# Kernel tuning notes

Hardware: AMD Instinct MI355X
Metric: run time of the kernel (lower is better)

The kernel has to match this reference:

```python
import jax, jax.numpy as jnp
import numpy as np

DIM = 1024
N_HEADS = 16
HEAD_DIM = DIM // N_HEADS


def setup_inputs() -> dict:
    key = jax.random.key(0)
    ks = jax.random.split(key, 5)
    x = jax.random.normal(ks[0], (2, 2048, DIM), dtype=jnp.float32)
    # nn.Linear-style init scale
    s = 1.0 / np.sqrt(DIM)
    W_qkv = jax.random.uniform(ks[1], (DIM, 3 * DIM), jnp.float32, -s, s)
    b_qkv = jax.random.uniform(ks[2], (3 * DIM,), jnp.float32, -s, s)
    W_proj = jax.random.uniform(ks[3], (DIM, DIM), jnp.float32, -s, s)
    b_proj = jax.random.uniform(ks[4], (DIM,), jnp.float32, -s, s)
    return {"x": x, "W_qkv": W_qkv, "b_qkv": b_qkv, "W_proj": W_proj, "b_proj": b_proj}


def reference(x, W_qkv, b_qkv, W_proj, b_proj):
    B, S, D = x.shape
    scale = HEAD_DIM ** -0.5
    qkv = x @ W_qkv + b_qkv                                   # [B,S,3D]
    qkv = qkv.reshape(B, S, 3, N_HEADS, HEAD_DIM)
    q = qkv[:, :, 0].transpose(0, 2, 1, 3)                    # [B,H,S,d]
    k = qkv[:, :, 1].transpose(0, 2, 1, 3)
    v = qkv[:, :, 2].transpose(0, 2, 1, 3)
    attn = jnp.einsum('bhqd,bhkd->bhqk', q, k) * scale        # [B,H,S,S]
    attn = jax.nn.softmax(attn, axis=-1)
    out = jnp.einsum('bhqk,bhkd->bhqd', attn, v)              # [B,H,S,d]
    out = out.transpose(0, 2, 1, 3).reshape(B, S, D)
    return out @ W_proj + b_proj
```

## Files before the change

kernel.cpp:

```cpp
#include <hip/hip_runtime.h>
#include <stdint.h>

typedef unsigned short u16;
typedef __attribute__((ext_vector_type(8))) short bf16x8;
typedef __attribute__((ext_vector_type(4))) float f32x4;
typedef __attribute__((ext_vector_type(16))) float f32x16;
typedef __attribute__((ext_vector_type(4))) u16 us4;
typedef __attribute__((ext_vector_type(8))) u16 us8;

__device__ __forceinline__ u16 f2bf(float f) {
  union { float f; unsigned u; } v; v.f = f;
  unsigned r = v.u + 0x7fffu + ((v.u >> 16) & 1u);
  return (u16)(r >> 16);
}

__device__ __forceinline__ float bf2f(u16 b) {
  union { float f; unsigned u; } v; v.u = ((unsigned)b) << 16;
  return v.f;
}

__device__ __forceinline__ unsigned pkbf(float a, float b) {
  union { float f; unsigned u; } x, y; x.f = a; y.f = b;
  return __builtin_amdgcn_perm(y.u + 0x8000u, x.u + 0x8000u, 0x07060302u);
}

__device__ __forceinline__ float fast_exp2(float x) {
#if __has_builtin(__builtin_amdgcn_exp2f)
  return __builtin_amdgcn_exp2f(x);
#else
  return exp2f(x);
#endif
}

__device__ __forceinline__ void gld16(const void* g, void* l) {
  __builtin_amdgcn_global_load_lds(
      (const __attribute__((address_space(1))) void*)g,
      (__attribute__((address_space(3))) void*)l, 16, 0, 0);
}

__global__ void cvt_kernel(const float* __restrict__ in, u16* __restrict__ out, int n4) {
  int i = blockIdx.x * blockDim.x + threadIdx.x;
  if (i >= n4) return;
  f32x4 v = ((const f32x4*)in)[i];
  us4 r;
#pragma unroll
  for (int j = 0; j < 4; ++j) r[j] = f2bf(v[j]);
  ((us4*)out)[i] = r;
}

__global__ void transw_kernel(const float* __restrict__ in, u16* __restrict__ out, int R, int C) {
  __shared__ u16 tile[32][33];
  const int tx = threadIdx.x & 31, ty = threadIdx.x >> 5;
  const int c0 = blockIdx.x * 32, r0 = blockIdx.y * 32;
#pragma unroll
  for (int j = 0; j < 4; ++j)
    tile[ty + j * 8][tx] = f2bf(in[(size_t)(r0 + ty + j * 8) * C + c0 + tx]);
  __syncthreads();
#pragma unroll
  for (int j = 0; j < 4; ++j)
    out[(size_t)(c0 + ty + j * 8) * R + r0 + tx] = tile[tx][ty + j * 8];
}

__global__ __launch_bounds__(256) void qkv_gemm_kernel(
    const u16* __restrict__ A, const u16* __restrict__ Bt, const float* __restrict__ bias,
    u16* __restrict__ Qb, u16* __restrict__ Kb, u16* __restrict__ Vtb) {
  __shared__ u16 sm[17408];
  u16* As = sm;
  u16* Bs = sm + 4096;
  const int tid = threadIdx.x;
  const int w = tid >> 6, l = tid & 63, quad = l >> 4, lanelo = l & 15;
  const int wr = w >> 1, wc = w & 1;
  const long m0 = (long)blockIdx.x * 128;
  const long n0 = (long)blockIdx.y * 128;

  f32x4 acc[4][4];
#pragma unroll
  for (int i = 0; i < 4; ++i)
#pragma unroll
    for (int j = 0; j < 4; ++j) acc[i][j] = (f32x4){0.f, 0.f, 0.f, 0.f};

  const u16* ag = A + (m0 + w * 32 + (l >> 2)) * 1024 + (l & 3) * 8;
  const u16* bg = Bt + (n0 + w * 32 + (l >> 2)) * 1024 + (l & 3) * 8;
  u16* asl = As + w * 1024;
  u16* bsl = Bs + w * 1024;

  for (int kt = 0; kt < 32; ++kt) {
    const int ko = kt * 32;
    gld16(ag + ko, asl);
    gld16(ag + 16 * 1024 + ko, asl + 512);
    gld16(bg + ko, bsl);
    gld16(bg + 16 * 1024 + ko, bsl + 512);
    __syncthreads();
    bf16x8 af[4], bf[4];
#pragma unroll
    for (int mt = 0; mt < 4; ++mt)
      af[mt] = *(const bf16x8*)(As + (wr * 64 + mt * 16 + lanelo) * 32 + quad * 8);
#pragma unroll
    for (int nt = 0; nt < 4; ++nt)
      bf[nt] = *(const bf16x8*)(Bs + (wc * 64 + nt * 16 + lanelo) * 32 + quad * 8);
#pragma unroll
    for (int mt = 0; mt < 4; ++mt)
#pragma unroll
      for (int nt = 0; nt < 4; ++nt)
        acc[mt][nt] = __builtin_amdgcn_mfma_f32_16x16x32_bf16(af[mt], bf[nt], acc[mt][nt], 0, 0, 0);
    __syncthreads();
  }

  const int t = (int)(n0 >> 10);
  const float scl = (t == 0) ? 0.18033688011112042f : 1.0f;

  float bias_v[4];
#pragma unroll
  for (int nt = 0; nt < 4; ++nt) bias_v[nt] = bias[n0 + wc * 64 + nt * 16 + lanelo];

  u16* Ct = sm;
#pragma unroll
  for (int mt = 0; mt < 4; ++mt)
#pragma unroll
    for (int nt = 0; nt < 4; ++nt)
#pragma unroll
      for (int r = 0; r < 4; ++r)
        Ct[(wr * 64 + mt * 16 + quad * 4 + r) * 136 + wc * 64 + nt * 16 + lanelo] =
            f2bf((acc[mt][nt][r] + bias_v[nt]) * scl);
  __syncthreads();

  const int b = (int)(m0 >> 11);
  const int s0 = (int)(m0 & 2047);
  const int h0 = (int)((n0 & 1023) >> 6);

  if (t < 2) {
    u16* dst = (t == 0) ? Qb : Kb;
#pragma unroll
    for (int p = 0; p < 8; ++p) {
      const int hh = p >> 2;
      const int sl = (p & 3) * 32 + (tid >> 3);
      const int c8 = tid & 7;
      us8 v = *(const us8*)(Ct + sl * 136 + hh * 64 + c8 * 8);
      const int pos = (c8 + sl) & 7;
      const size_t off = ((size_t)((b * 16 + h0 + hh) * 2048 + s0 + sl)) * 64 + pos * 8;
      *(us8*)(dst + off) = v;
    }
  } else {
#pragma unroll
    for (int p = 0; p < 8; ++p) {
      const int hh = p >> 2;
      const int dl = (p & 3) * 16 + (tid >> 4);
      const int c16 = tid & 15;
      us8 v;
#pragma unroll
      for (int j = 0; j < 8; ++j) v[j] = Ct[(c16 * 8 + j) * 136 + hh * 64 + dl];
      const int pos = (c16 + dl) & 15;
      const size_t off = ((size_t)((b * 16 + h0 + hh) * 64 + dl)) * 2048 + s0 + pos * 8;
      *(us8*)(Vtb + off) = v;
    }
  }
}

__global__ __launch_bounds__(256, 4) void attn_kernel(
    const u16* __restrict__ Qb, const u16* __restrict__ Kb,
    const u16* __restrict__ Vtb, u16* __restrict__ Op, float* __restrict__ lp) {
  __shared__ u16 Ks[8192];
  __shared__ u16 Vs[8192];
  const int tid = threadIdx.x;
  const int w = tid >> 6, l = tid & 63;
  const int m = l & 31, hi = l >> 5;
  const int qt = blockIdx.x, head = blockIdx.y, z = blockIdx.z;
  const u16* Qh = Qb + (size_t)head * 2048 * 64;
  const u16* Kh = Kb + (size_t)head * 2048 * 64;
  const u16* Vh = Vtb + (size_t)head * 64 * 2048;
  const int permaddr = (l ^ 32) << 2;

  const int qrow = qt * 128 + w * 32 + m;
  bf16x8 qf[4];
#pragma unroll
  for (int ks = 0; ks < 4; ++ks) {
    const int c = ks * 2 + hi;
    const int pos = (c + qrow) & 7;
    qf[ks] = *(const bf16x8*)(Qh + (size_t)qrow * 64 + pos * 8);
  }

  f32x16 o0, o1;
#pragma unroll
  for (int i = 0; i < 16; ++i) { o0[i] = 0.f; o1[i] = 0.f; }
  float sacc = 0.f;

  for (int kt = 0; kt < 8; ++kt) {
    const int kb = z * 8 + kt;
    const u16* kbase = Kh + (size_t)kb * 8192;
#pragma unroll
    for (int j = 0; j < 4; ++j) {
      const int i = w * 4 + j;
      gld16(kbase + i * 512 + l * 8, &Ks[i * 512]);
    }
#pragma unroll
    for (int j = 0; j < 4; ++j) {
      const int i = w * 4 + j;
      const int dd = i * 4 + (l >> 4);
      gld16(Vh + (size_t)dd * 2048 + kb * 128 + (l & 15) * 8, &Vs[i * 512]);
    }
    __syncthreads();

#pragma unroll
    for (int g = 0; g < 4; ++g) {
      f32x16 st;
#pragma unroll
      for (int i = 0; i < 16; ++i) st[i] = 0.f;
      const int key = g * 32 + m;
#pragma unroll
      for (int ks = 0; ks < 4; ++ks) {
        const int c = ks * 2 + hi;
        const int pos = (c + key) & 7;
        bf16x8 kf = *(const bf16x8*)(&Ks[key * 64 + pos * 8]);
        st = __builtin_amdgcn_mfma_f32_32x32x16_bf16(kf, qf[ks], st, 0, 0, 0);
      }

      float p[16];
#pragma unroll
      for (int r = 0; r < 16; ++r) p[r] = fast_exp2(st[r]);
#pragma unroll
      for (int r = 0; r < 16; ++r) sacc += p[r];

      unsigned L[8];
#pragma unroll
      for (int q4 = 0; q4 < 4; ++q4) {
        L[2 * q4] = pkbf(p[4 * q4], p[4 * q4 + 1]);
        L[2 * q4 + 1] = pkbf(p[4 * q4 + 2], p[4 * q4 + 3]);
      }

#pragma unroll
      for (int s = 0; s < 2; ++s) {
        const unsigned a0 = L[4 * s], a1 = L[4 * s + 1];
        const unsigned b0 = L[4 * s + 2], b1 = L[4 * s + 3];
        const unsigned s0 = hi ? a0 : b0;
        const unsigned s1 = hi ? a1 : b1;
        const unsigned r0 = (unsigned)__builtin_amdgcn_ds_bpermute(permaddr, (int)s0);
        const unsigned r1 = (unsigned)__builtin_amdgcn_ds_bpermute(permaddr, (int)s1);
        int4 fd;
        fd.x = (int)(hi ? r0 : a0);
        fd.y = (int)(hi ? r1 : a1);
        fd.z = (int)(hi ? b0 : r0);
        fd.w = (int)(hi ? b1 : r1);
        union { int4 i; bf16x8 v; } pu; pu.i = fd;
        const int c = g * 4 + s * 2 + hi;
#pragma unroll
        for (int n = 0; n < 2; ++n) {
          const int d = n * 32 + m;
          const int pos = (c + d) & 15;
          bf16x8 vf = *(const bf16x8*)(&Vs[d * 128 + pos * 8]);
          if (n == 0) o0 = __builtin_amdgcn_mfma_f32_32x32x16_bf16(pu.v, vf, o0, 0, 0, 0);
          else        o1 = __builtin_amdgcn_mfma_f32_32x32x16_bf16(pu.v, vf, o1, 0, 0, 0);
        }
      }
    }
    __syncthreads();
  }

  union { float f; int i; } sv; sv.f = sacc;
  union { float f; int i; } pv; pv.i = __builtin_amdgcn_ds_bpermute(permaddr, sv.i);
  const float ltot = sacc + pv.f;
  if (hi == 0)
    lp[(size_t)z * 65536 + (size_t)head * 2048 + qt * 128 + w * 32 + m] = ltot;

  const int b = head >> 4, h = head & 15;
  u16* Od = Op + (size_t)z * 4194304;
#pragma unroll
  for (int r = 0; r < 16; ++r) {
    const int qlocal = (r & 3) + 8 * (r >> 2) + 4 * hi;
    const size_t base =
        ((size_t)(b * 2048 + qt * 128 + w * 32 + qlocal)) * 1024 + h * 64;
    Od[base + m] = f2bf(o0[r]);
    Od[base + 32 + m] = f2bf(o1[r]);
  }
}

__global__ __launch_bounds__(128) void combine_kernel(
    const u16* __restrict__ Op, const float* __restrict__ lp, u16* __restrict__ Ob) {
  const int r = blockIdx.x;
  const int tid = threadIdx.x;
  const int col = tid * 8;
  const int b = r >> 11, s = r & 2047, h = col >> 6;
  const size_t li = (size_t)(b * 16 + h) * 2048 + s;
  const float linv = 1.0f / (lp[li] + lp[65536 + li]);
  us8 v0 = *(const us8*)(Op + (size_t)r * 1024 + col);
  us8 v1 = *(const us8*)(Op + 4194304 + (size_t)r * 1024 + col);
  us8 o;
#pragma unroll
  for (int j = 0; j < 8; ++j)
    o[j] = f2bf((bf2f(v0[j]) + bf2f(v1[j])) * linv);
  *(us8*)(Ob + (size_t)r * 1024 + col) = o;
}

__global__ __launch_bounds__(256) void proj_gemm_kernel(
    const u16* __restrict__ A, const u16* __restrict__ Bt,
    const float* __restrict__ bias, float* __restrict__ out) {
  __shared__ u16 sm[8192];
  u16* As = sm;
  u16* Bs = sm + 4096;
  const int tid = threadIdx.x;
  const int w = tid >> 6, l = tid & 63, quad = l >> 4, lanelo = l & 15;
  const int wr = w >> 1, wc = w & 1;
  const long m0 = (long)blockIdx.x * 128;
  const long n0 = (long)blockIdx.y * 128;
  const int z = blockIdx.z;

  f32x4 acc[4][4];
#pragma unroll
  for (int i = 0; i < 4; ++i)
#pragma unroll
    for (int j = 0; j < 4; ++j) acc[i][j] = (f32x4){0.f, 0.f, 0.f, 0.f};

  const u16* ag = A + (m0 + w * 32 + (l >> 2)) * 1024 + z * 512 + (l & 3) * 8;
  const u16* bg = Bt + (n0 + w * 32 + (l >> 2)) * 1024 + z * 512 + (l & 3) * 8;
  u16* asl = As + w * 1024;
  u16* bsl = Bs + w * 1024;

  for (int kt = 0; kt < 16; ++kt) {
    const int ko = kt * 32;
    gld16(ag + ko, asl);
    gld16(ag + 16 * 1024 + ko, asl + 512);
    gld16(bg + ko, bsl);
    gld16(bg + 16 * 1024 + ko, bsl + 512);
    __syncthreads();
    bf16x8 af[4], bf[4];
#pragma unroll
    for (int mt = 0; mt < 4; ++mt)
      af[mt] = *(const bf16x8*)(As + (wr * 64 + mt * 16 + lanelo) * 32 + quad * 8);
#pragma unroll
    for (int nt = 0; nt < 4; ++nt)
      bf[nt] = *(const bf16x8*)(Bs + (wc * 64 + nt * 16 + lanelo) * 32 + quad * 8);
#pragma unroll
    for (int mt = 0; mt < 4; ++mt)
#pragma unroll
      for (int nt = 0; nt < 4; ++nt)
        acc[mt][nt] = __builtin_amdgcn_mfma_f32_16x16x32_bf16(af[mt], bf[nt], acc[mt][nt], 0, 0, 0);
    __syncthreads();
  }

  float bias_v[4];
#pragma unroll
  for (int nt = 0; nt < 4; ++nt)
    bias_v[nt] = z ? 0.f : bias[n0 + wc * 64 + nt * 16 + lanelo];

#pragma unroll
  for (int mt = 0; mt < 4; ++mt)
#pragma unroll
    for (int nt = 0; nt < 4; ++nt)
#pragma unroll
      for (int r = 0; r < 4; ++r) {
        const size_t mm = m0 + wr * 64 + mt * 16 + quad * 4 + r;
        const size_t nn = n0 + wc * 64 + nt * 16 + lanelo;
        atomicAdd(&out[mm * 1024 + nn], acc[mt][nt][r] + bias_v[nt]);
      }
}

extern "C" void kernel_launch(void* const* d_in, const int* in_sizes, int n_in,
                              void* d_out, int out_size, void* d_ws, size_t ws_size,
                              hipStream_t stream) {
  const float* x = (const float*)d_in[0];
  const float* Wqkv = (const float*)d_in[1];
  const float* bqkv = (const float*)d_in[2];
  const float* Wproj = (const float*)d_in[3];
  const float* bproj = (const float*)d_in[4];
  float* out = (float*)d_out;
  char* ws = (char*)d_ws;

  u16* Xb   = (u16*)(ws);
  u16* Op   = (u16*)(ws);
  u16* Wqkt = (u16*)(ws + 8388608);
  u16* Qb   = (u16*)(ws + 16777216);
  u16* Ob   = (u16*)(ws + 16777216);
  u16* Kb   = (u16*)(ws + 25165824);
  u16* Vtb  = (u16*)(ws + 33554432);
  u16* Wpt  = (u16*)(ws + 41943040);
  float* lp = (float*)(ws + 44040192);

  hipMemsetAsync(out, 0, (size_t)4096 * 1024 * 4, stream);

  cvt_kernel<<<4096, 256, 0, stream>>>(x, Xb, 1048576);
  transw_kernel<<<dim3(96, 32), 256, 0, stream>>>(Wqkv, Wqkt, 1024, 3072);
  transw_kernel<<<dim3(32, 32), 256, 0, stream>>>(Wproj, Wpt, 1024, 1024);
  qkv_gemm_kernel<<<dim3(32, 24), 256, 0, stream>>>(Xb, Wqkt, bqkv, Qb, Kb, Vtb);
  attn_kernel<<<dim3(16, 32, 2), 256, 0, stream>>>(Qb, Kb, Vtb, Op, lp);
  combine_kernel<<<4096, 128, 0, stream>>>(Op, lp, Ob);
  proj_gemm_kernel<<<dim3(32, 8, 2), 256, 0, stream>>>(Ob, Wpt, bproj, out);
}
```

Measured before the change: 218.7 us.

## Remap GEMM blocks per XCD, MFMA row sums, drop split-K atomics in proj

The QKV and projection GEMMs now remap their block indices so that blocks landing on the same XCD share A/B tiles, which is meant to improve L2 reuse. The attention kernel computes the softmax row sums with an extra MFMA against a ones vector, replacing the scalar adds and the cross-lane permute. The projection GEMM drops its split-K with atomics in favour of 128x64 tiles over the full K and plain stores, which also removes the output memset. This trades fewer atomics and one launch for longer per-block K loops and one additional MFMA per P fragment.

```diff
diff --git a/kernel.cpp b/kernel.cpp
--- a/kernel.cpp
+++ b/kernel.cpp
@@ -70,8 +70,10 @@
   const int tid = threadIdx.x;
   const int w = tid >> 6, l = tid & 63, quad = l >> 4, lanelo = l & 15;
   const int wr = w >> 1, wc = w & 1;
-  const long m0 = (long)blockIdx.x * 128;
-  const long n0 = (long)blockIdx.y * 128;
+  const int flat = blockIdx.x + 32 * blockIdx.y;
+  const int xcd = flat & 7, lid = flat >> 3;
+  const long m0 = (long)((xcd >> 1) * 8 + (lid & 7)) * 128;
+  const long n0 = (long)((xcd & 1) * 12 + (lid >> 3)) * 128;
 
   f32x4 acc[4][4];
 #pragma unroll
@@ -179,10 +181,12 @@
     qf[ks] = *(const bf16x8*)(Qh + (size_t)qrow * 64 + pos * 8);
   }
 
-  f32x16 o0, o1;
-#pragma unroll
-  for (int i = 0; i < 16; ++i) { o0[i] = 0.f; o1[i] = 0.f; }
-  float sacc = 0.f;
+  f32x16 o0, o1, os32;
+#pragma unroll
+  for (int i = 0; i < 16; ++i) { o0[i] = 0.f; o1[i] = 0.f; os32[i] = 0.f; }
+  bf16x8 ones;
+#pragma unroll
+  for (int j = 0; j < 8; ++j) ones[j] = (short)0x3F80;
 
   for (int kt = 0; kt < 8; ++kt) {
     const int kb = z * 8 + kt;
@@ -217,8 +221,6 @@
       float p[16];
 #pragma unroll
       for (int r = 0; r < 16; ++r) p[r] = fast_exp2(st[r]);
-#pragma unroll
-      for (int r = 0; r < 16; ++r) sacc += p[r];
 
       unsigned L[8];
 #pragma unroll
@@ -241,6 +243,7 @@
         fd.z = (int)(hi ? b0 : r0);
         fd.w = (int)(hi ? b1 : r1);
         union { int4 i; bf16x8 v; } pu; pu.i = fd;
+        os32 = __builtin_amdgcn_mfma_f32_32x32x16_bf16(pu.v, ones, os32, 0, 0, 0);
         const int c = g * 4 + s * 2 + hi;
 #pragma unroll
         for (int n = 0; n < 2; ++n) {
@@ -255,11 +258,13 @@
     __syncthreads();
   }
 
-  union { float f; int i; } sv; sv.f = sacc;
-  union { float f; int i; } pv; pv.i = __builtin_amdgcn_ds_bpermute(permaddr, sv.i);
-  const float ltot = sacc + pv.f;
-  if (hi == 0)
-    lp[(size_t)z * 65536 + (size_t)head * 2048 + qt * 128 + w * 32 + m] = ltot;
+  if (m == 0) {
+#pragma unroll
+    for (int r = 0; r < 16; ++r) {
+      const int q = (r & 3) + 8 * (r >> 2) + 4 * hi;
+      lp[(size_t)z * 65536 + (size_t)head * 2048 + qt * 128 + w * 32 + q] = os32[r];
+    }
+  }
 
   const int b = head >> 4, h = head & 15;
   u16* Od = Op + (size_t)z * 4194304;
@@ -293,63 +298,63 @@
 __global__ __launch_bounds__(256) void proj_gemm_kernel(
     const u16* __restrict__ A, const u16* __restrict__ Bt,
     const float* __restrict__ bias, float* __restrict__ out) {
-  __shared__ u16 sm[8192];
+  __shared__ u16 sm[6144];
   u16* As = sm;
   u16* Bs = sm + 4096;
   const int tid = threadIdx.x;
   const int w = tid >> 6, l = tid & 63, quad = l >> 4, lanelo = l & 15;
   const int wr = w >> 1, wc = w & 1;
-  const long m0 = (long)blockIdx.x * 128;
-  const long n0 = (long)blockIdx.y * 128;
-  const int z = blockIdx.z;
-
-  f32x4 acc[4][4];
+  const int flat = blockIdx.x + 32 * blockIdx.y;
+  const int xcd = flat & 7, lid = flat >> 3;
+  const long m0 = (long)(xcd * 4 + (lid & 3)) * 128;
+  const long n0 = (long)(lid >> 2) * 64;
+
+  f32x4 acc[4][2];
 #pragma unroll
   for (int i = 0; i < 4; ++i)
 #pragma unroll
-    for (int j = 0; j < 4; ++j) acc[i][j] = (f32x4){0.f, 0.f, 0.f, 0.f};
-
-  const u16* ag = A + (m0 + w * 32 + (l >> 2)) * 1024 + z * 512 + (l & 3) * 8;
-  const u16* bg = Bt + (n0 + w * 32 + (l >> 2)) * 1024 + z * 512 + (l & 3) * 8;
+    for (int j = 0; j < 2; ++j) acc[i][j] = (f32x4){0.f, 0.f, 0.f, 0.f};
+
+  const u16* ag = A + (m0 + w * 32 + (l >> 2)) * 1024 + (l & 3) * 8;
+  const u16* bg = Bt + (n0 + w * 16 + (l >> 2)) * 1024 + (l & 3) * 8;
   u16* asl = As + w * 1024;
-  u16* bsl = Bs + w * 1024;
-
-  for (int kt = 0; kt < 16; ++kt) {
+  u16* bsl = Bs + w * 512;
+
+  for (int kt = 0; kt < 32; ++kt) {
     const int ko = kt * 32;
     gld16(ag + ko, asl);
     gld16(ag + 16 * 1024 + ko, asl + 512);
     gld16(bg + ko, bsl);
-    gld16(bg + 16 * 1024 + ko, bsl + 512);
-    __syncthreads();
-    bf16x8 af[4], bf[4];
+    __syncthreads();
+    bf16x8 af[4], bf[2];
 #pragma unroll
     for (int mt = 0; mt < 4; ++mt)
       af[mt] = *(const bf16x8*)(As + (wr * 64 + mt * 16 + lanelo) * 32 + quad * 8);
 #pragma unroll
-    for (int nt = 0; nt < 4; ++nt)
-      bf[nt] = *(const bf16x8*)(Bs + (wc * 64 + nt * 16 + lanelo) * 32 + quad * 8);
+    for (int nt = 0; nt < 2; ++nt)
+      bf[nt] = *(const bf16x8*)(Bs + (wc * 32 + nt * 16 + lanelo) * 32 + quad * 8);
 #pragma unroll
     for (int mt = 0; mt < 4; ++mt)
 #pragma unroll
-      for (int nt = 0; nt < 4; ++nt)
+      for (int nt = 0; nt < 2; ++nt)
         acc[mt][nt] = __builtin_amdgcn_mfma_f32_16x16x32_bf16(af[mt], bf[nt], acc[mt][nt], 0, 0, 0);
     __syncthreads();
   }
 
-  float bias_v[4];
-#pragma unroll
-  for (int nt = 0; nt < 4; ++nt)
-    bias_v[nt] = z ? 0.f : bias[n0 + wc * 64 + nt * 16 + lanelo];
+  float bias_v[2];
+#pragma unroll
+  for (int nt = 0; nt < 2; ++nt)
+    bias_v[nt] = bias[n0 + wc * 32 + nt * 16 + lanelo];
 
 #pragma unroll
   for (int mt = 0; mt < 4; ++mt)
 #pragma unroll
-    for (int nt = 0; nt < 4; ++nt)
+    for (int nt = 0; nt < 2; ++nt)
 #pragma unroll
       for (int r = 0; r < 4; ++r) {
         const size_t mm = m0 + wr * 64 + mt * 16 + quad * 4 + r;
-        const size_t nn = n0 + wc * 64 + nt * 16 + lanelo;
-        atomicAdd(&out[mm * 1024 + nn], acc[mt][nt][r] + bias_v[nt]);
+        const size_t nn = n0 + wc * 32 + nt * 16 + lanelo;
+        out[mm * 1024 + nn] = acc[mt][nt][r] + bias_v[nt];
       }
 }
 
@@ -374,13 +379,11 @@
   u16* Wpt  = (u16*)(ws + 41943040);
   float* lp = (float*)(ws + 44040192);
 
-  hipMemsetAsync(out, 0, (size_t)4096 * 1024 * 4, stream);
-
   cvt_kernel<<<4096, 256, 0, stream>>>(x, Xb, 1048576);
   transw_kernel<<<dim3(96, 32), 256, 0, stream>>>(Wqkv, Wqkt, 1024, 3072);
   transw_kernel<<<dim3(32, 32), 256, 0, stream>>>(Wproj, Wpt, 1024, 1024);
   qkv_gemm_kernel<<<dim3(32, 24), 256, 0, stream>>>(Xb, Wqkt, bqkv, Qb, Kb, Vtb);
   attn_kernel<<<dim3(16, 32, 2), 256, 0, stream>>>(Qb, Kb, Vtb, Op, lp);
   combine_kernel<<<4096, 128, 0, stream>>>(Op, lp, Ob);
-  proj_gemm_kernel<<<dim3(32, 8, 2), 256, 0, stream>>>(Ob, Wpt, bproj, out);
-}
+  proj_gemm_kernel<<<dim3(32, 16), 256, 0, stream>>>(Ob, Wpt, bproj, out);
+}
```

Result: faster. 193.5 us (-11.5%).

## Retile attention and projection, add XCD-aware block remap, drop split-K atomics

Applied to the files above, without the earlier changes.

Attention blocks shrink to 2 waves over 64 queries with 64-key tiles, which doubles the block count. The V-transpose store layout in the QKV GEMM changes to match the new 64-wide key tiles. Block indices in the QKV GEMM, attention and projection kernels are remapped so neighbouring tiles land on the same XCD, aiming at better L2 reuse. The projection GEMM moves from 128x128 split-K with atomics to 64x64 tiles with 32x32 MFMA and plain stores, which removes the output memset and the atomic traffic but leaves less reuse per tile.

```diff
diff --git a/kernel.cpp b/kernel.cpp
--- a/kernel.cpp
+++ b/kernel.cpp
@@ -70,8 +70,10 @@
   const int tid = threadIdx.x;
   const int w = tid >> 6, l = tid & 63, quad = l >> 4, lanelo = l & 15;
   const int wr = w >> 1, wc = w & 1;
-  const long m0 = (long)blockIdx.x * 128;
-  const long n0 = (long)blockIdx.y * 128;
+  const int flat = blockIdx.x + 32 * blockIdx.y;
+  const int xcd = flat & 7, lid = flat >> 3;
+  const long m0 = (long)((xcd >> 1) * 8 + (lid & 7)) * 128;
+  const long n0 = (long)((xcd & 1) * 12 + (lid >> 3)) * 128;
 
   f32x4 acc[4][4];
 #pragma unroll
@@ -149,28 +151,32 @@
       us8 v;
 #pragma unroll
       for (int j = 0; j < 8; ++j) v[j] = Ct[(c16 * 8 + j) * 136 + hh * 64 + dl];
-      const int pos = (c16 + dl) & 15;
-      const size_t off = ((size_t)((b * 16 + h0 + hh) * 64 + dl)) * 2048 + s0 + pos * 8;
+      const int sub = c16 >> 3, c8 = c16 & 7;
+      const int pos = (c8 + dl) & 7;
+      const size_t off = ((size_t)((b * 16 + h0 + hh) * 64 + dl)) * 2048 + s0 + sub * 64 + pos * 8;
       *(us8*)(Vtb + off) = v;
     }
   }
 }
 
-__global__ __launch_bounds__(256, 4) void attn_kernel(
+__global__ __launch_bounds__(128, 4) void attn_kernel(
     const u16* __restrict__ Qb, const u16* __restrict__ Kb,
     const u16* __restrict__ Vtb, u16* __restrict__ Op, float* __restrict__ lp) {
-  __shared__ u16 Ks[8192];
-  __shared__ u16 Vs[8192];
+  __shared__ u16 Ks[4096];
+  __shared__ u16 Vs[4096];
   const int tid = threadIdx.x;
   const int w = tid >> 6, l = tid & 63;
   const int m = l & 31, hi = l >> 5;
-  const int qt = blockIdx.x, head = blockIdx.y, z = blockIdx.z;
+  const int fid = blockIdx.x + 32 * (blockIdx.y + 32 * blockIdx.z);
+  const int head = (fid & 7) + 8 * ((fid >> 3) & 3);
+  const int qt = (fid >> 5) & 31;
+  const int z = fid >> 10;
   const u16* Qh = Qb + (size_t)head * 2048 * 64;
   const u16* Kh = Kb + (size_t)head * 2048 * 64;
   const u16* Vh = Vtb + (size_t)head * 64 * 2048;
   const int permaddr = (l ^ 32) << 2;
 
-  const int qrow = qt * 128 + w * 32 + m;
+  const int qrow = qt * 64 + w * 32 + m;
   bf16x8 qf[4];
 #pragma unroll
   for (int ks = 0; ks < 4; ++ks) {
@@ -184,9 +190,10 @@
   for (int i = 0; i < 16; ++i) { o0[i] = 0.f; o1[i] = 0.f; }
   float sacc = 0.f;
 
-  for (int kt = 0; kt < 8; ++kt) {
-    const int kb = z * 8 + kt;
-    const u16* kbase = Kh + (size_t)kb * 8192;
+  const u16* kbase = Kh + (size_t)(z * 1024) * 64;
+  const u16* vbase = Vh + z * 1024;
+
+  for (int t = 0; t < 16; ++t) {
 #pragma unroll
     for (int j = 0; j < 4; ++j) {
       const int i = w * 4 + j;
@@ -195,13 +202,13 @@
 #pragma unroll
     for (int j = 0; j < 4; ++j) {
       const int i = w * 4 + j;
-      const int dd = i * 4 + (l >> 4);
-      gld16(Vh + (size_t)dd * 2048 + kb * 128 + (l & 15) * 8, &Vs[i * 512]);
-    }
-    __syncthreads();
-
-#pragma unroll
-    for (int g = 0; g < 4; ++g) {
+      const int dd = i * 8 + (l >> 3);
+      gld16(vbase + (size_t)dd * 2048 + (l & 7) * 8, &Vs[i * 512]);
+    }
+    __syncthreads();
+
+#pragma unroll
+    for (int g = 0; g < 2; ++g) {
       f32x16 st;
 #pragma unroll
       for (int i = 0; i < 16; ++i) st[i] = 0.f;
@@ -245,21 +252,23 @@
 #pragma unroll
         for (int n = 0; n < 2; ++n) {
           const int d = n * 32 + m;
-          const int pos = (c + d) & 15;
-          bf16x8 vf = *(const bf16x8*)(&Vs[d * 128 + pos * 8]);
+          const int pos = (c + d) & 7;
+          bf16x8 vf = *(const bf16x8*)(&Vs[d * 64 + pos * 8]);
           if (n == 0) o0 = __builtin_amdgcn_mfma_f32_32x32x16_bf16(pu.v, vf, o0, 0, 0, 0);
           else        o1 = __builtin_amdgcn_mfma_f32_32x32x16_bf16(pu.v, vf, o1, 0, 0, 0);
         }
       }
     }
     __syncthreads();
+    kbase += 4096;
+    vbase += 64;
   }
 
   union { float f; int i; } sv; sv.f = sacc;
   union { float f; int i; } pv; pv.i = __builtin_amdgcn_ds_bpermute(permaddr, sv.i);
   const float ltot = sacc + pv.f;
   if (hi == 0)
-    lp[(size_t)z * 65536 + (size_t)head * 2048 + qt * 128 + w * 32 + m] = ltot;
+    lp[(size_t)z * 65536 + (size_t)head * 2048 + qt * 64 + w * 32 + m] = ltot;
 
   const int b = head >> 4, h = head & 15;
   u16* Od = Op + (size_t)z * 4194304;
@@ -267,7 +276,7 @@
   for (int r = 0; r < 16; ++r) {
     const int qlocal = (r & 3) + 8 * (r >> 2) + 4 * hi;
     const size_t base =
-        ((size_t)(b * 2048 + qt * 128 + w * 32 + qlocal)) * 1024 + h * 64;
+        ((size_t)(b * 2048 + qt * 64 + w * 32 + qlocal)) * 1024 + h * 64;
     Od[base + m] = f2bf(o0[r]);
     Od[base + 32 + m] = f2bf(o1[r]);
   }
@@ -293,64 +302,50 @@
 __global__ __launch_bounds__(256) void proj_gemm_kernel(
     const u16* __restrict__ A, const u16* __restrict__ Bt,
     const float* __restrict__ bias, float* __restrict__ out) {
-  __shared__ u16 sm[8192];
+  __shared__ u16 sm[4096];
   u16* As = sm;
-  u16* Bs = sm + 4096;
+  u16* Bs = sm + 2048;
   const int tid = threadIdx.x;
-  const int w = tid >> 6, l = tid & 63, quad = l >> 4, lanelo = l & 15;
-  const int wr = w >> 1, wc = w & 1;
-  const long m0 = (long)blockIdx.x * 128;
-  const long n0 = (long)blockIdx.y * 128;
-  const int z = blockIdx.z;
-
-  f32x4 acc[4][4];
-#pragma unroll
-  for (int i = 0; i < 4; ++i)
-#pragma unroll
-    for (int j = 0; j < 4; ++j) acc[i][j] = (f32x4){0.f, 0.f, 0.f, 0.f};
-
-  const u16* ag = A + (m0 + w * 32 + (l >> 2)) * 1024 + z * 512 + (l & 3) * 8;
-  const u16* bg = Bt + (n0 + w * 32 + (l >> 2)) * 1024 + z * 512 + (l & 3) * 8;
-  u16* asl = As + w * 1024;
-  u16* bsl = Bs + w * 1024;
-
-  for (int kt = 0; kt < 16; ++kt) {
+  const int w = tid >> 6, l = tid & 63;
+  const int m = l & 31, hi = l >> 5;
+  const int wy = w >> 1, wx = w & 1;
+  const int flat = blockIdx.x + 64 * blockIdx.y;
+  const int xcd = flat & 7, lid = flat >> 3;
+  const long m0 = (long)(xcd * 8 + (lid >> 4)) * 64;
+  const long n0 = (long)(lid & 15) * 64;
+
+  f32x16 acc;
+#pragma unroll
+  for (int i = 0; i < 16; ++i) acc[i] = 0.f;
+
+  const u16* ag = A + (m0 + (tid >> 2)) * 1024 + (tid & 3) * 8;
+  const u16* bg = Bt + (n0 + (tid >> 2)) * 1024 + (tid & 3) * 8;
+  u16* asl = As + w * 512;
+  u16* bsl = Bs + w * 512;
+
+  for (int kt = 0; kt < 32; ++kt) {
     const int ko = kt * 32;
     gld16(ag + ko, asl);
-    gld16(ag + 16 * 1024 + ko, asl + 512);
     gld16(bg + ko, bsl);
-    gld16(bg + 16 * 1024 + ko, bsl + 512);
-    __syncthreads();
-    bf16x8 af[4], bf[4];
-#pragma unroll
-    for (int mt = 0; mt < 4; ++mt)
-      af[mt] = *(const bf16x8*)(As + (wr * 64 + mt * 16 + lanelo) * 32 + quad * 8);
-#pragma unroll
-    for (int nt = 0; nt < 4; ++nt)
-      bf[nt] = *(const bf16x8*)(Bs + (wc * 64 + nt * 16 + lanelo) * 32 + quad * 8);
-#pragma unroll
-    for (int mt = 0; mt < 4; ++mt)
-#pragma unroll
-      for (int nt = 0; nt < 4; ++nt)
-        acc[mt][nt] = __builtin_amdgcn_mfma_f32_16x16x32_bf16(af[mt], bf[nt], acc[mt][nt], 0, 0, 0);
-    __syncthreads();
-  }
-
-  float bias_v[4];
-#pragma unroll
-  for (int nt = 0; nt < 4; ++nt)
-    bias_v[nt] = z ? 0.f : bias[n0 + wc * 64 + nt * 16 + lanelo];
-
-#pragma unroll
-  for (int mt = 0; mt < 4; ++mt)
-#pragma unroll
-    for (int nt = 0; nt < 4; ++nt)
-#pragma unroll
-      for (int r = 0; r < 4; ++r) {
-        const size_t mm = m0 + wr * 64 + mt * 16 + quad * 4 + r;
-        const size_t nn = n0 + wc * 64 + nt * 16 + lanelo;
-        atomicAdd(&out[mm * 1024 + nn], acc[mt][nt][r] + bias_v[nt]);
-      }
+    __syncthreads();
+    bf16x8 af[2], bf[2];
+#pragma unroll
+    for (int ks = 0; ks < 2; ++ks) {
+      af[ks] = *(const bf16x8*)(As + (wy * 32 + m) * 32 + ks * 16 + hi * 8);
+      bf[ks] = *(const bf16x8*)(Bs + (wx * 32 + m) * 32 + ks * 16 + hi * 8);
+    }
+    acc = __builtin_amdgcn_mfma_f32_32x32x16_bf16(af[0], bf[0], acc, 0, 0, 0);
+    acc = __builtin_amdgcn_mfma_f32_32x32x16_bf16(af[1], bf[1], acc, 0, 0, 0);
+    __syncthreads();
+  }
+
+  const float bias_v = bias[n0 + wx * 32 + m];
+#pragma unroll
+  for (int r = 0; r < 16; ++r) {
+    const size_t mm = m0 + wy * 32 + (r & 3) + 8 * (r >> 2) + 4 * hi;
+    const size_t nn = n0 + wx * 32 + m;
+    out[mm * 1024 + nn] = acc[r] + bias_v;
+  }
 }
 
 extern "C" void kernel_launch(void* const* d_in, const int* in_sizes, int n_in,
@@ -374,13 +369,11 @@
   u16* Wpt  = (u16*)(ws + 41943040);
   float* lp = (float*)(ws + 44040192);
 
-  hipMemsetAsync(out, 0, (size_t)4096 * 1024 * 4, stream);
-
   cvt_kernel<<<4096, 256, 0, stream>>>(x, Xb, 1048576);
   transw_kernel<<<dim3(96, 32), 256, 0, stream>>>(Wqkv, Wqkt, 1024, 3072);
   transw_kernel<<<dim3(32, 32), 256, 0, stream>>>(Wproj, Wpt, 1024, 1024);
   qkv_gemm_kernel<<<dim3(32, 24), 256, 0, stream>>>(Xb, Wqkt, bqkv, Qb, Kb, Vtb);
-  attn_kernel<<<dim3(16, 32, 2), 256, 0, stream>>>(Qb, Kb, Vtb, Op, lp);
+  attn_kernel<<<dim3(32, 32, 2), 128, 0, stream>>>(Qb, Kb, Vtb, Op, lp);
   combine_kernel<<<4096, 128, 0, stream>>>(Op, lp, Ob);
-  proj_gemm_kernel<<<dim3(32, 8, 2), 256, 0, stream>>>(Ob, Wpt, bproj, out);
-}
+  proj_gemm_kernel<<<dim3(64, 16), 256, 0, stream>>>(Ob, Wpt, bproj, out);
+}
```

Result: faster. 205.1 us (-6.2%).
